# Kernel optimization log

Measured on AMD Instinct MI355X. Metric: run time of the kernel, lower is better.

Reference implementation:

```python
import jax, jax.numpy as jnp
import numpy as np

# ProjectorConfig defaults
MIN_SPEECH_FRAMES = 1.0
MAX_SPEECH_EXPAND = 3.0
TAIL_HOLD_UNITS = 2
BOUNDARY_COMMIT_THRESHOLD = 0.45

B, U = 4096, 2048


def setup_inputs() -> dict:
    key = jax.random.key(0)
    ks = jax.random.split(key, 10)
    # ragged prefix mask: random visible length per row (faithful to streaming use)
    lengths = jax.random.randint(ks[0], (B,), 1, U + 1)
    unit_mask = (jnp.arange(U)[None, :] < lengths[:, None]).astype(jnp.float32)
    dur_anchor_src = jax.random.uniform(ks[1], (B, U), jnp.float32) * 20.0
    dur_logratio_unit = jax.random.normal(ks[2], (B, U), jnp.float32) * 0.3
    pause_weight_unit = jax.random.uniform(ks[3], (B, U), jnp.float32)
    boundary_latent = jax.random.uniform(ks[4], (B, U), jnp.float32)
    speech_budget_win = jax.random.uniform(ks[5], (B, 1), jnp.float32) * float(U) * 10.0
    pause_budget_win = jax.random.uniform(ks[6], (B, 1), jnp.float32) * float(U)
    open_run_mask = jax.random.bernoulli(ks[7], 0.1, (B, U)).astype(jnp.int32)
    return {
        "dur_anchor_src": dur_anchor_src,
        "unit_mask": unit_mask,
        "speech_budget_win": speech_budget_win,
        "pause_budget_win": pause_budget_win,
        "dur_logratio_unit": dur_logratio_unit,
        "pause_weight_unit": pause_weight_unit,
        "boundary_latent": boundary_latent,
        "phase_ptr": jnp.zeros((B,), jnp.float32),
        "backlog": jnp.zeros((B,), jnp.float32),
        "clock_delta": jnp.zeros((B,), jnp.float32),
        "commit_frontier": jnp.zeros((B,), jnp.int32),
        "open_run_mask": open_run_mask,
    }


def reference(dur_anchor_src, unit_mask, speech_budget_win, pause_budget_win,
              dur_logratio_unit, pause_weight_unit, boundary_latent,
              phase_ptr, backlog, clock_delta, commit_frontier, open_run_mask):
    b, u = unit_mask.shape

    # ---- _project_speech ----
    anchor = jnp.maximum(dur_anchor_src, MIN_SPEECH_FRAMES)
    base = anchor * jnp.exp(dur_logratio_unit)
    speech = jnp.maximum(jnp.minimum(base, anchor * MAX_SPEECH_EXPAND), MIN_SPEECH_FRAMES) * unit_mask
    total = jnp.maximum((speech * unit_mask).sum(axis=1, keepdims=True), 1e-6)
    speech = speech * (speech_budget_win / total) * unit_mask

    # ---- _project_pause ----
    scores = jnp.maximum(pause_weight_unit, 0.0) * (0.5 + boundary_latent) * unit_mask
    score_total = scores.sum(axis=1, keepdims=True)
    fallback = unit_mask / jnp.maximum(unit_mask.sum(axis=1, keepdims=True), 1.0)
    weights = jnp.where(score_total > 0, scores / jnp.maximum(score_total, 1e-6), fallback)
    pause = weights * pause_budget_win

    effective = (speech + pause) * unit_mask

    # ---- _compute_commit_frontier (vectorized) ----
    visible = unit_mask.sum(axis=1).astype(jnp.int32)                 # active_len [B]
    idx = jnp.arange(u, dtype=jnp.int32)[None, :]
    open_vis = (open_run_mask > 0) & (idx < visible[:, None])
    has_open = open_vis.any(axis=1)
    first_open = jnp.argmax(open_vis, axis=1).astype(jnp.int32)
    closed_prefix = jnp.where(has_open, first_open, visible)          # leading closed run
    release_cap = jnp.maximum(visible - TAIL_HOLD_UNITS, 0)
    candidate = jnp.minimum(release_cap, closed_prefix)
    prev = commit_frontier.astype(jnp.int32)
    b_idx = jnp.clip(candidate - 1, 0, u - 1)
    b_val = jnp.take_along_axis(boundary_latent, b_idx[:, None], axis=1)[:, 0]
    soft = (candidate > 0) & (candidate < visible) & (b_val < BOUNDARY_COMMIT_THRESHOLD)
    candidate = jnp.where(soft, jnp.maximum(prev, candidate - 1), candidate)
    commit = jnp.maximum(prev, candidate)

    # ---- _advance_state (prefix sums instead of python loops) ----
    zeros_col = jnp.zeros((b, 1), effective.dtype)
    cs_eff = jnp.concatenate([zeros_col, jnp.cumsum(effective, axis=1)], axis=1)
    cs_src = jnp.concatenate([zeros_col, jnp.cumsum(dur_anchor_src, axis=1)], axis=1)
    take = lambda cs, i: jnp.take_along_axis(cs, i[:, None], axis=1)[:, 0]
    exec_prefix = take(cs_eff, commit) - take(cs_eff, prev)
    src_prefix = take(cs_src, commit) - take(cs_src, prev)
    adv = commit > prev
    delta = exec_prefix - src_prefix
    next_clock = jnp.where(adv, clock_delta + delta, clock_delta)
    next_backlog = jnp.where(adv, jnp.maximum(next_clock, 0.0), backlog)
    visible_total = jnp.maximum(effective.sum(axis=1), 1.0)
    next_phase = jnp.where(adv, jnp.clip(phase_ptr + exec_prefix / visible_total, 0.0, 1.0), phase_ptr)

    return (speech, pause, effective, commit, next_phase, next_backlog, next_clock)
```

## Files before the change

kernel.cpp:

```cpp
#include <hip/hip_runtime.h>
#include <climits>


constexpr int UNITS = 2048;
constexpr int BLOCK = 256;

typedef float f32x4 __attribute__((ext_vector_type(4)));

static __device__ __forceinline__ float waveSum(float v) {
#pragma unroll
  for (int m = 1; m < 64; m <<= 1) v += __shfl_xor(v, m, 64);
  return v;
}

__global__ __launch_bounds__(BLOCK, 4) void rhythm_kernel(
    const float* __restrict__ dur_anchor,
    const float* __restrict__ unit_mask,
    const float* __restrict__ speech_budget,
    const float* __restrict__ pause_budget,
    const float* __restrict__ dur_logratio,
    const float* __restrict__ pause_weight,
    const float* __restrict__ boundary,
    const float* __restrict__ phase_ptr,
    const float* __restrict__ backlog,
    const float* __restrict__ clock_delta,
    const int*   __restrict__ commit_front,
    const int*   __restrict__ open_run,
    float* __restrict__ out,
    int B) {
  const int row = blockIdx.x;
  const int t = threadIdx.x;
  const int wv = t >> 6, ln = t & 63;
  const size_t base = (size_t)row * UNITS;

  const int prev = commit_front[row];
  const float sb = speech_budget[row];
  const float pb = pause_budget[row];
  const float pp = phase_ptr[row];
  const float bl = backlog[row];
  const float cd = clock_delta[row];

  int visible;
  {
    const int i = (ln < 32) ? ln : 0;
    const float v1 = unit_mask[base + 64 * i + 63];
    const int c1 = __popcll(__ballot((ln < 32) && (v1 > 0.5f)));
    if (c1 == 32) {
      visible = 2048;
    } else {
      const int s = 64 * c1;
      const float v2 = unit_mask[base + s + ln];
      visible = s + __popcll(__ballot(v2 > 0.5f));
    }
  }

  int min_open = INT_MAX;
  for (int cs = 0; cs < visible; cs += 256) {
    const int e = cs + 4 * ln;
    int4 o4 = make_int4(0, 0, 0, 0);
    if (e < visible) o4 = *(const int4*)(open_run + base + e);
    int lm = INT_MAX;
    if (o4.w > 0 && e + 3 < visible) lm = e + 3;
    if (o4.z > 0 && e + 2 < visible) lm = e + 2;
    if (o4.y > 0 && e + 1 < visible) lm = e + 1;
    if (o4.x > 0 && e < visible) lm = e;
    const unsigned long long bb = __ballot(lm != INT_MAX);
    if (bb) {
      const int l0 = (int)__ffsll(bb) - 1;
      min_open = __shfl(lm, l0, 64);
      break;
    }
  }

  float sv_sr[8];
  float sv_sc[8];
  float sv_a[2][4] = {};
  (void)sv_a;
  float sum_sr = 0.f, sum_sc = 0.f;

#pragma unroll
  for (int c = 0; c < 2; ++c) {
    const int e0 = c * 1024 + 4 * t;
    if (e0 < visible) {
      const float4 a4 = *(const float4*)(dur_anchor   + base + e0);
      const float4 l4 = *(const float4*)(dur_logratio + base + e0);
      const float4 p4 = *(const float4*)(pause_weight + base + e0);
      const float4 b4 = *(const float4*)(boundary     + base + e0);
      const float av[4] = {a4.x, a4.y, a4.z, a4.w};
      const float lv[4] = {l4.x, l4.y, l4.z, l4.w};
      const float pv[4] = {p4.x, p4.y, p4.z, p4.w};
      const float bv[4] = {b4.x, b4.y, b4.z, b4.w};
#pragma unroll
      for (int j = 0; j < 4; ++j) {
        const int k = c * 4 + j;
        const float m = (e0 + j < visible) ? 1.0f : 0.0f;
        const float a = fmaxf(av[j], 1.0f);
        const float bse = a * __expf(lv[j]);
        const float sr = fmaxf(fminf(bse, 3.0f * a), 1.0f) * m;
        const float sc = fmaxf(pv[j], 0.0f) * (0.5f + bv[j]) * m;
        sv_sr[k] = sr;
        sv_sc[k] = sc;
        sum_sr += sr;
        sum_sc += sc;
      }
    } else {
#pragma unroll
      for (int j = 0; j < 4; ++j) { sv_sr[c * 4 + j] = 0.f; sv_sc[c * 4 + j] = 0.f; }
    }
  }

  __shared__ float sf[2][4];
  __shared__ float sg[2][4];
  const float r0 = waveSum(sum_sr);
  const float r1 = waveSum(sum_sc);
  if (ln == 0) { sf[0][wv] = r0; sf[1][wv] = r1; }
  __syncthreads();

  const float ts = sf[0][0] + sf[0][1] + sf[0][2] + sf[0][3];
  const float tc = sf[1][0] + sf[1][1] + sf[1][2] + sf[1][3];
  const float tm = (float)visible;

  const int closed = (min_open == INT_MAX) ? visible : min_open;
  const int relcap = max(visible - 2, 0);
  int cand = min(relcap, closed);
  const int bidx = min(max(cand - 1, 0), UNITS - 1);
  const float bval = boundary[base + bidx];
  if (cand > 0 && cand < visible && bval < 0.45f)
    cand = max(prev, cand - 1);
  const int commit = max(prev, cand);

  const float sscale = sb / fmaxf(ts, 1e-6f);
  const bool usefb = !(tc > 0.0f);
  const float pscale = pb / fmaxf(tc, 1e-6f);
  const float fbw = pb / fmaxf(tm, 1.0f);
  const float eff_tot = usefb ? (sscale * ts + fbw * tm) : (sscale * ts + pscale * tc);

  float src_rng = 0.f;
  for (int i = prev + t; i < commit; i += BLOCK) src_rng += dur_anchor[base + i];

  float* __restrict__ out_speech = out;
  float* __restrict__ out_pause  = out + (size_t)B * UNITS;
  float* __restrict__ out_eff    = out + 2 * (size_t)B * UNITS;

  float eff_rng = 0.f;
#pragma unroll
  for (int c = 0; c < 2; ++c) {
    const int e0 = c * 1024 + 4 * t;
    f32x4 s4, q4, e4;
#pragma unroll
    for (int j = 0; j < 4; ++j) {
      const int k = c * 4 + j;
      const int idx = e0 + j;
      const float m = (idx < visible) ? 1.0f : 0.0f;
      const float speech = sv_sr[k] * sscale;
      const float pause = usefb ? (m * fbw) : (sv_sc[k] * pscale);
      const float eff = (speech + pause) * m;
      s4[j] = speech;
      q4[j] = pause;
      e4[j] = eff;
      const bool inr = (idx >= prev) && (idx < commit);
      eff_rng += inr ? eff : 0.f;
    }
    __builtin_nontemporal_store(s4, (f32x4*)(out_speech + base + e0));
    __builtin_nontemporal_store(q4, (f32x4*)(out_pause + base + e0));
    __builtin_nontemporal_store(e4, (f32x4*)(out_eff + base + e0));
  }

  const float q0 = waveSum(eff_rng);
  const float q1 = waveSum(src_rng);
  if (ln == 0) { sg[0][wv] = q0; sg[1][wv] = q1; }
  __syncthreads();

  if (t == 0) {
    const float execp = sg[0][0] + sg[0][1] + sg[0][2] + sg[0][3];
    const float srcp  = sg[1][0] + sg[1][1] + sg[1][2] + sg[1][3];
    const bool adv = commit > prev;
    const float nclock = adv ? (cd + (execp - srcp)) : cd;
    const float nback = adv ? fmaxf(nclock, 0.0f) : bl;
    const float vt = fmaxf(eff_tot, 1.0f);
    const float nphase =
        adv ? fminf(fmaxf(pp + execp / vt, 0.0f), 1.0f) : pp;
    const size_t o = 3 * (size_t)B * UNITS;
    out[o + row] = (float)commit;
    out[o + (size_t)B + row] = nphase;
    out[o + 2 * (size_t)B + row] = nback;
    out[o + 3 * (size_t)B + row] = nclock;
  }
}

extern "C" void kernel_launch(void* const* d_in, const int* in_sizes, int n_in,
                              void* d_out, int out_size, void* d_ws, size_t ws_size,
                              hipStream_t stream) {
  const int B = in_sizes[7];
  rhythm_kernel<<<dim3(B), dim3(BLOCK), 0, stream>>>(
      (const float*)d_in[0],
      (const float*)d_in[1],
      (const float*)d_in[2],
      (const float*)d_in[3],
      (const float*)d_in[4],
      (const float*)d_in[5],
      (const float*)d_in[6],
      (const float*)d_in[7],
      (const float*)d_in[8],
      (const float*)d_in[9],
      (const int*)d_in[10],
      (const int*)d_in[11],
      (float*)d_out, B);
}
```

Before: 244.8 us.

## Split row kernel into wave-per-row stats pass and separate elementwise write pass

The single block-per-row kernel is replaced by two kernels. A stats kernel gives each row to one wavefront, computes the sums, commit and scalar state, and also the in-range effective sum directly from the inputs, then writes per-row scale parameters to workspace. A second kernel with two blocks per row reloads the four inputs and writes speech, pause and effective outputs. This removes block-level syncs and shared-memory reductions, but the inputs are read twice and a second launch is added.

After: 252.3 us. +3.0%, slower.

```diff
diff --git a/kernel.cpp b/kernel.cpp
--- a/kernel.cpp
+++ b/kernel.cpp
@@ -3,17 +3,16 @@
 
 
 constexpr int UNITS = 2048;
-constexpr int BLOCK = 256;
 
 typedef float f32x4 __attribute__((ext_vector_type(4)));
 
-static __device__ __forceinline__ float waveSum(float v) {
+static __device__ __forceinline__ float bflySum(float v) {
 #pragma unroll
   for (int m = 1; m < 64; m <<= 1) v += __shfl_xor(v, m, 64);
   return v;
 }
 
-__global__ __launch_bounds__(BLOCK, 4) void rhythm_kernel(
+__global__ __launch_bounds__(256, 4) void stats_kernel(
     const float* __restrict__ dur_anchor,
     const float* __restrict__ unit_mask,
     const float* __restrict__ speech_budget,
@@ -27,10 +26,11 @@
     const int*   __restrict__ commit_front,
     const int*   __restrict__ open_run,
     float* __restrict__ out,
+    float4* __restrict__ params,
     int B) {
-  const int row = blockIdx.x;
-  const int t = threadIdx.x;
-  const int wv = t >> 6, ln = t & 63;
+  const int wv = threadIdx.x >> 6, ln = threadIdx.x & 63;
+  const int row = blockIdx.x * 4 + wv;
+  if (row >= B) return;
   const size_t base = (size_t)row * UNITS;
 
   const int prev = commit_front[row];
@@ -66,58 +66,36 @@
     if (o4.x > 0 && e < visible) lm = e;
     const unsigned long long bb = __ballot(lm != INT_MAX);
     if (bb) {
-      const int l0 = (int)__ffsll(bb) - 1;
-      min_open = __shfl(lm, l0, 64);
+      min_open = __shfl(lm, (int)__ffsll((unsigned long long)bb) - 1, 64);
       break;
     }
   }
 
-  float sv_sr[8];
-  float sv_sc[8];
-  float sv_a[2][4] = {};
-  (void)sv_a;
   float sum_sr = 0.f, sum_sc = 0.f;
-
-#pragma unroll
-  for (int c = 0; c < 2; ++c) {
-    const int e0 = c * 1024 + 4 * t;
-    if (e0 < visible) {
-      const float4 a4 = *(const float4*)(dur_anchor   + base + e0);
-      const float4 l4 = *(const float4*)(dur_logratio + base + e0);
-      const float4 p4 = *(const float4*)(pause_weight + base + e0);
-      const float4 b4 = *(const float4*)(boundary     + base + e0);
+  for (int cs = 0; cs < visible; cs += 256) {
+    const int e = cs + 4 * ln;
+    if (e < visible) {
+      const float4 a4 = *(const float4*)(dur_anchor   + base + e);
+      const float4 l4 = *(const float4*)(dur_logratio + base + e);
+      const float4 p4 = *(const float4*)(pause_weight + base + e);
+      const float4 b4 = *(const float4*)(boundary     + base + e);
       const float av[4] = {a4.x, a4.y, a4.z, a4.w};
       const float lv[4] = {l4.x, l4.y, l4.z, l4.w};
       const float pv[4] = {p4.x, p4.y, p4.z, p4.w};
       const float bv[4] = {b4.x, b4.y, b4.z, b4.w};
 #pragma unroll
       for (int j = 0; j < 4; ++j) {
-        const int k = c * 4 + j;
-        const float m = (e0 + j < visible) ? 1.0f : 0.0f;
+        const float m = (e + j < visible) ? 1.0f : 0.0f;
         const float a = fmaxf(av[j], 1.0f);
-        const float bse = a * __expf(lv[j]);
-        const float sr = fmaxf(fminf(bse, 3.0f * a), 1.0f) * m;
+        const float sr = fmaxf(fminf(a * __expf(lv[j]), 3.0f * a), 1.0f) * m;
         const float sc = fmaxf(pv[j], 0.0f) * (0.5f + bv[j]) * m;
-        sv_sr[k] = sr;
-        sv_sc[k] = sc;
         sum_sr += sr;
         sum_sc += sc;
       }
-    } else {
-#pragma unroll
-      for (int j = 0; j < 4; ++j) { sv_sr[c * 4 + j] = 0.f; sv_sc[c * 4 + j] = 0.f; }
-    }
-  }
-
-  __shared__ float sf[2][4];
-  __shared__ float sg[2][4];
-  const float r0 = waveSum(sum_sr);
-  const float r1 = waveSum(sum_sc);
-  if (ln == 0) { sf[0][wv] = r0; sf[1][wv] = r1; }
-  __syncthreads();
-
-  const float ts = sf[0][0] + sf[0][1] + sf[0][2] + sf[0][3];
-  const float tc = sf[1][0] + sf[1][1] + sf[1][2] + sf[1][3];
+    }
+  }
+  const float ts = bflySum(sum_sr);
+  const float tc = bflySum(sum_sc);
   const float tm = (float)visible;
 
   const int closed = (min_open == INT_MAX) ? visible : min_open;
@@ -133,47 +111,25 @@
   const bool usefb = !(tc > 0.0f);
   const float pscale = pb / fmaxf(tc, 1e-6f);
   const float fbw = pb / fmaxf(tm, 1.0f);
+  const float pm = usefb ? fbw : pscale;
   const float eff_tot = usefb ? (sscale * ts + fbw * tm) : (sscale * ts + pscale * tc);
 
-  float src_rng = 0.f;
-  for (int i = prev + t; i < commit; i += BLOCK) src_rng += dur_anchor[base + i];
-
-  float* __restrict__ out_speech = out;
-  float* __restrict__ out_pause  = out + (size_t)B * UNITS;
-  float* __restrict__ out_eff    = out + 2 * (size_t)B * UNITS;
-
-  float eff_rng = 0.f;
-#pragma unroll
-  for (int c = 0; c < 2; ++c) {
-    const int e0 = c * 1024 + 4 * t;
-    f32x4 s4, q4, e4;
-#pragma unroll
-    for (int j = 0; j < 4; ++j) {
-      const int k = c * 4 + j;
-      const int idx = e0 + j;
-      const float m = (idx < visible) ? 1.0f : 0.0f;
-      const float speech = sv_sr[k] * sscale;
-      const float pause = usefb ? (m * fbw) : (sv_sc[k] * pscale);
-      const float eff = (speech + pause) * m;
-      s4[j] = speech;
-      q4[j] = pause;
-      e4[j] = eff;
-      const bool inr = (idx >= prev) && (idx < commit);
-      eff_rng += inr ? eff : 0.f;
-    }
-    __builtin_nontemporal_store(s4, (f32x4*)(out_speech + base + e0));
-    __builtin_nontemporal_store(q4, (f32x4*)(out_pause + base + e0));
-    __builtin_nontemporal_store(e4, (f32x4*)(out_eff + base + e0));
-  }
-
-  const float q0 = waveSum(eff_rng);
-  const float q1 = waveSum(src_rng);
-  if (ln == 0) { sg[0][wv] = q0; sg[1][wv] = q1; }
-  __syncthreads();
-
-  if (t == 0) {
-    const float execp = sg[0][0] + sg[0][1] + sg[0][2] + sg[0][3];
-    const float srcp  = sg[1][0] + sg[1][1] + sg[1][2] + sg[1][3];
+  float src_rng = 0.f, eff_rng = 0.f;
+  for (int i = prev + ln; i < commit; i += 64) {
+    const float a = dur_anchor[base + i];
+    const float l = dur_logratio[base + i];
+    const float p = pause_weight[base + i];
+    const float bo = boundary[base + i];
+    src_rng += a;
+    const float aa = fmaxf(a, 1.0f);
+    const float sr = fmaxf(fminf(aa * __expf(l), 3.0f * aa), 1.0f);
+    const float sc = fmaxf(p, 0.0f) * (0.5f + bo);
+    eff_rng += sr * sscale + (usefb ? pm : sc * pm);
+  }
+  const float srcp = bflySum(src_rng);
+  const float execp = bflySum(eff_rng);
+
+  if (ln == 0) {
     const bool adv = commit > prev;
     const float nclock = adv ? (cd + (execp - srcp)) : cd;
     const float nback = adv ? fmaxf(nclock, 0.0f) : bl;
@@ -185,25 +141,72 @@
     out[o + (size_t)B + row] = nphase;
     out[o + 2 * (size_t)B + row] = nback;
     out[o + 3 * (size_t)B + row] = nclock;
-  }
+    params[row] = make_float4((float)visible, sscale, pm, usefb ? 1.0f : 0.0f);
+  }
+}
+
+__global__ __launch_bounds__(256, 4) void write_kernel(
+    const float* __restrict__ dur_anchor,
+    const float* __restrict__ dur_logratio,
+    const float* __restrict__ pause_weight,
+    const float* __restrict__ boundary,
+    const float4* __restrict__ params,
+    float* __restrict__ out, int B) {
+  const int row = blockIdx.x >> 1;
+  const int half = blockIdx.x & 1;
+  const int e0 = half * 1024 + 4 * threadIdx.x;
+  const size_t base = (size_t)row * UNITS;
+
+  const float4 pr = params[row];
+  const int visible = (int)pr.x;
+  const float sscale = pr.y;
+  const float pm = pr.z;
+  const bool usefb = pr.w != 0.0f;
+
+  f32x4 s4 = {0.f, 0.f, 0.f, 0.f}, q4 = {0.f, 0.f, 0.f, 0.f},
+        e4 = {0.f, 0.f, 0.f, 0.f};
+  if (e0 < visible) {
+    const float4 a4 = *(const float4*)(dur_anchor   + base + e0);
+    const float4 l4 = *(const float4*)(dur_logratio + base + e0);
+    const float4 p4 = *(const float4*)(pause_weight + base + e0);
+    const float4 b4 = *(const float4*)(boundary     + base + e0);
+    const float av[4] = {a4.x, a4.y, a4.z, a4.w};
+    const float lv[4] = {l4.x, l4.y, l4.z, l4.w};
+    const float pv[4] = {p4.x, p4.y, p4.z, p4.w};
+    const float bv[4] = {b4.x, b4.y, b4.z, b4.w};
+#pragma unroll
+    for (int j = 0; j < 4; ++j) {
+      const float m = (e0 + j < visible) ? 1.0f : 0.0f;
+      const float a = fmaxf(av[j], 1.0f);
+      const float sr = fmaxf(fminf(a * __expf(lv[j]), 3.0f * a), 1.0f);
+      const float sc = fmaxf(pv[j], 0.0f) * (0.5f + bv[j]);
+      const float speech = sr * sscale * m;
+      const float pause = (usefb ? pm : sc * pm) * m;
+      s4[j] = speech;
+      q4[j] = pause;
+      e4[j] = speech + pause;
+    }
+  }
+  float* __restrict__ out_speech = out;
+  float* __restrict__ out_pause  = out + (size_t)B * UNITS;
+  float* __restrict__ out_eff    = out + 2 * (size_t)B * UNITS;
+  __builtin_nontemporal_store(s4, (f32x4*)(out_speech + base + e0));
+  __builtin_nontemporal_store(q4, (f32x4*)(out_pause + base + e0));
+  __builtin_nontemporal_store(e4, (f32x4*)(out_eff + base + e0));
 }
 
 extern "C" void kernel_launch(void* const* d_in, const int* in_sizes, int n_in,
                               void* d_out, int out_size, void* d_ws, size_t ws_size,
                               hipStream_t stream) {
   const int B = in_sizes[7];
-  rhythm_kernel<<<dim3(B), dim3(BLOCK), 0, stream>>>(
-      (const float*)d_in[0],
-      (const float*)d_in[1],
-      (const float*)d_in[2],
-      (const float*)d_in[3],
-      (const float*)d_in[4],
-      (const float*)d_in[5],
-      (const float*)d_in[6],
-      (const float*)d_in[7],
-      (const float*)d_in[8],
-      (const float*)d_in[9],
-      (const int*)d_in[10],
-      (const int*)d_in[11],
-      (float*)d_out, B);
-}
+  float4* params = (float4*)d_ws;
+  stats_kernel<<<dim3((B + 3) / 4), dim3(256), 0, stream>>>(
+      (const float*)d_in[0], (const float*)d_in[1], (const float*)d_in[2],
+      (const float*)d_in[3], (const float*)d_in[4], (const float*)d_in[5],
+      (const float*)d_in[6], (const float*)d_in[7], (const float*)d_in[8],
+      (const float*)d_in[9], (const int*)d_in[10], (const int*)d_in[11],
+      (float*)d_out, params, B);
+  write_kernel<<<dim3(2 * B), dim3(256), 0, stream>>>(
+      (const float*)d_in[0], (const float*)d_in[4], (const float*)d_in[5],
+      (const float*)d_in[6], params, (float*)d_out, B);
+}
```
